# Kernel tuning notes

Measured on AMD Instinct MI355X. Metric: run time of the kernel, lower is better.

## Reference

```python
import jax, jax.numpy as jnp
import numpy as np

B, S, D, H = 4, 2048, 1024, 16
DK = D // H

def setup_inputs() -> dict:
    key = jax.random.key(0)
    ks = jax.random.split(key, 11)
    sc = 1.0 / np.sqrt(D)
    return {
        "query": jax.random.normal(ks[0], (B, S, D), jnp.float32),
        "key_": jax.random.normal(ks[1], (B, S, D), jnp.float32),
        "value": jax.random.normal(ks[2], (B, S, D), jnp.float32),
        "Wq": jax.random.normal(ks[3], (D, D), jnp.float32) * sc,
        "bq": jnp.zeros((D,), jnp.float32),
        "Wk": jax.random.normal(ks[4], (D, D), jnp.float32) * sc,
        "bk": jnp.zeros((D,), jnp.float32),
        "Wv": jax.random.normal(ks[5], (D, D), jnp.float32) * sc,
        "bv": jnp.zeros((D,), jnp.float32),
        "Wo": jax.random.normal(ks[6], (D, D), jnp.float32) * sc,
        "bo": jnp.zeros((D,), jnp.float32),
    }

def reference(query, key_, value, Wq, bq, Wk, bk, Wv, bv, Wo, bo):
    def proj(x, W, b):
        # [B,S,D] -> [B,H,S,DK]
        y = x @ W.T + b
        return y.reshape(B, S, H, DK).transpose(0, 2, 1, 3)
    q = proj(query, Wq, bq)
    k = proj(key_, Wk, bk)
    v = proj(value, Wv, bv)
    scores = jnp.einsum("bhqd,bhkd->bhqk", q, k) / jnp.sqrt(jnp.float32(DK))
    p = jax.nn.softmax(scores, axis=-1)
    x = jnp.einsum("bhqk,bhkd->bhqd", p, v)
    x = x.transpose(0, 2, 1, 3).reshape(B, S, D)
    return x @ Wo.T + bo
```

## Files before the change

kernel.cpp:

```cpp
#include <hip/hip_runtime.h>
#include <math.h>

#define Bc 4
#define Sc 2048
#define Dc 1024
#define Hc 16
#define DKc 64

#define QSCALE_L2E 0.1803368801f
#define ZINIT_L2E  -11.5415603f

typedef __bf16 bf16;
typedef __bf16 bf16x2 __attribute__((ext_vector_type(2)));
typedef __bf16 bf16x4 __attribute__((ext_vector_type(4)));
typedef __bf16 bf16x8 __attribute__((ext_vector_type(8)));
typedef float  floatx4 __attribute__((ext_vector_type(4)));
typedef float  floatx16 __attribute__((ext_vector_type(16)));

__device__ __forceinline__ void load_lds16(const void* g, void* l) {
    __builtin_amdgcn_global_load_lds((const __attribute__((address_space(1))) void*)g,
                                     (__attribute__((address_space(3))) void*)l, 16, 0, 0);
}

#define MFMA16(a, b, c) __builtin_amdgcn_mfma_f32_16x16x32_bf16(a, b, c, 0, 0, 0)
#define MFMA32(a, b, c) __builtin_amdgcn_mfma_f32_32x32x16_bf16(a, b, c, 0, 0, 0)

__device__ __forceinline__ float exp2_fast(float x) {
    float r;
    asm("v_exp_f32 %0, %1" : "=v"(r) : "v"(x));
    return r;
}


#define GSTAGE(dbuf, kk) do {                                                 \
    load_lds16(A + (size_t)(m0 + w * 16 + srow) * K + (kk) + scol,            \
               As + (dbuf) * 4096 + w * 512);                                 \
    load_lds16(W + (size_t)(n0 + w * 16 + srow) * K + (kk) + scol,            \
               Bs + (dbuf) * 4096 + w * 512);                                 \
    load_lds16(A + (size_t)(m0 + (w + 4) * 16 + srow) * K + (kk) + scol,      \
               As + (dbuf) * 4096 + (w + 4) * 512);                           \
    load_lds16(W + (size_t)(n0 + (w + 4) * 16 + srow) * K + (kk) + scol,      \
               Bs + (dbuf) * 4096 + (w + 4) * 512);                           \
} while (0)

#define GCOMP(dbuf) do {                                                      \
    const bf16* Ab = As + (dbuf) * 4096;                                      \
    const bf16* Bb = Bs + (dbuf) * 4096;                                      \
    const bf16x8 af0 = *(const bf16x8*)(Ab + (wm + fl) * 32 + fq * 8);        \
    const bf16x8 af1 = *(const bf16x8*)(Ab + (wm + 16 + fl) * 32 + fq * 8);   \
    const bf16x8 af2 = *(const bf16x8*)(Ab + (wm + 32 + fl) * 32 + fq * 8);   \
    const bf16x8 af3 = *(const bf16x8*)(Ab + (wm + 48 + fl) * 32 + fq * 8);   \
    const bf16x8 bg0 = *(const bf16x8*)(Bb + (wn + fl) * 32 + fq * 8);        \
    const bf16x8 bg1 = *(const bf16x8*)(Bb + (wn + 16 + fl) * 32 + fq * 8);   \
    const bf16x8 bg2 = *(const bf16x8*)(Bb + (wn + 32 + fl) * 32 + fq * 8);   \
    const bf16x8 bg3 = *(const bf16x8*)(Bb + (wn + 48 + fl) * 32 + fq * 8);   \
    acc[0][0] = MFMA16(af0, bg0, acc[0][0]); acc[0][1] = MFMA16(af0, bg1, acc[0][1]); \
    acc[0][2] = MFMA16(af0, bg2, acc[0][2]); acc[0][3] = MFMA16(af0, bg3, acc[0][3]); \
    acc[1][0] = MFMA16(af1, bg0, acc[1][0]); acc[1][1] = MFMA16(af1, bg1, acc[1][1]); \
    acc[1][2] = MFMA16(af1, bg2, acc[1][2]); acc[1][3] = MFMA16(af1, bg3, acc[1][3]); \
    acc[2][0] = MFMA16(af2, bg0, acc[2][0]); acc[2][1] = MFMA16(af2, bg1, acc[2][1]); \
    acc[2][2] = MFMA16(af2, bg2, acc[2][2]); acc[2][3] = MFMA16(af2, bg3, acc[2][3]); \
    acc[3][0] = MFMA16(af3, bg0, acc[3][0]); acc[3][1] = MFMA16(af3, bg1, acc[3][1]); \
    acc[3][2] = MFMA16(af3, bg2, acc[3][2]); acc[3][3] = MFMA16(af3, bg3, acc[3][3]); \
} while (0)

template<int MODE>
__device__ __forceinline__ void gemm_body(const bf16* __restrict__ A,
                                          const bf16* __restrict__ W,
                                          const float* __restrict__ bias,
                                          void* __restrict__ out,
                                          bf16* As, bf16* Bs,
                                          int m0, int n0) {
    constexpr int N = Dc, K = Dc;
    const int t  = threadIdx.x;
    const int w  = t >> 6;
    const int l  = t & 63;
    const int wm = (w >> 1) * 64;
    const int wn = (w & 1) * 64;
    const int srow = l >> 2;
    const int scol = (l & 3) * 8;
    const int fl = l & 15;
    const int fq = l >> 4;

    floatx4 acc[4][4];
#pragma unroll
    for (int i = 0; i < 4; i++)
#pragma unroll
        for (int j = 0; j < 4; j++)
            acc[i][j] = (floatx4){0.f, 0.f, 0.f, 0.f};

    GSTAGE(0, 0);
    __syncthreads();
#pragma unroll 1
    for (int k0 = 0; k0 < K; k0 += 64) {
        GSTAGE(1, k0 + 32);
        GCOMP(0);
        __syncthreads();
        if (k0 + 64 < K) GSTAGE(0, k0 + 64);
        GCOMP(1);
        __syncthreads();
    }

#pragma unroll
    for (int tn = 0; tn < 4; tn++) {
        const int n = n0 + wn + tn * 16 + fl;
        const float bv = bias[n];
#pragma unroll
        for (int tm = 0; tm < 4; tm++) {
            const int mb = m0 + wm + tm * 16 + fq * 4;
            if (MODE == 0) {
                float* O = (float*)out;
#pragma unroll
                for (int r = 0; r < 4; r++)
                    O[(size_t)(mb + r) * N + n] = acc[tm][tn][r] + bv;
            } else if (MODE == 1) {
                bf16* O = (bf16*)out;
#pragma unroll
                for (int r = 0; r < 4; r++)
                    O[(size_t)(mb + r) * N + n] = (bf16)(acc[tm][tn][r] + bv);
            } else {
                const int h = n >> 6, dk = n & 63;
                const int b = mb >> 11, s = mb & 2047;
                bf16* O = (bf16*)out + ((size_t)((b * Hc + h) * DKc + dk)) * Sc + s;
                bf16x4 pk = {(bf16)(acc[tm][tn][0] + bv), (bf16)(acc[tm][tn][1] + bv),
                             (bf16)(acc[tm][tn][2] + bv), (bf16)(acc[tm][tn][3] + bv)};
                *(bf16x4*)O = pk;
            }
        }
    }
}

__global__ __launch_bounds__(256) void gemm_qkv(
    const bf16* __restrict__ Aq, const bf16* __restrict__ Ak, const bf16* __restrict__ Av,
    const bf16* __restrict__ Wqb, const bf16* __restrict__ Wkb, const bf16* __restrict__ Wvb,
    const float* __restrict__ bqs, const float* __restrict__ bk, const float* __restrict__ bv,
    bf16* __restrict__ Oq, bf16* __restrict__ Ok, bf16* __restrict__ Ov) {
    __shared__ bf16 As[2 * 128 * 32];
    __shared__ bf16 Bs[2 * 128 * 32];
    const int bid  = blockIdx.x;
    const int xcd  = bid & 7;
    const int slot = bid >> 3;
    const int x    = slot & 7;
    const int j    = slot >> 3;
    const int yg   = xcd + 8 * j;
    const int sel  = yg >> 6;
    const int y    = yg & 63;
    const int m0 = y * 128, n0 = x * 128;
    if (sel == 0)      gemm_body<1>(Aq, Wqb, bqs, Oq, As, Bs, m0, n0);
    else if (sel == 1) gemm_body<1>(Ak, Wkb, bk,  Ok, As, Bs, m0, n0);
    else               gemm_body<2>(Av, Wvb, bv,  Ov, As, Bs, m0, n0);
}

__global__ __launch_bounds__(256) void gemm_out_k(const bf16* __restrict__ A,
                                                  const bf16* __restrict__ W,
                                                  const float* __restrict__ bias,
                                                  float* __restrict__ out) {
    __shared__ bf16 As[2 * 128 * 32];
    __shared__ bf16 Bs[2 * 128 * 32];
    const int bid  = blockIdx.x;
    const int xcd  = bid & 7;
    const int slot = bid >> 3;
    const int x    = slot & 7;
    const int j    = slot >> 3;
    const int y    = xcd + 8 * j;
    gemm_body<0>(A, W, bias, out, As, Bs, y * 128, x * 128);
}


__device__ __forceinline__ unsigned pkpair(float a, float b) {
    union { bf16x2 v; unsigned u; } x;
    x.v = (bf16x2){(bf16)a, (bf16)b};
    return x.u;
}

__device__ __forceinline__ bf16x8 frag4(unsigned a, unsigned b, unsigned c, unsigned d) {
    union { unsigned u[4]; bf16x8 v; } x;
    x.u[0] = a; x.u[1] = b; x.u[2] = c; x.u[3] = d;
    return x.v;
}

__device__ __forceinline__ floatx16 splat16(float v) {
    floatx16 r;
#pragma unroll
    for (int i = 0; i < 16; ++i) r[i] = v;
    return r;
}

#define PSWAP(x, y) do {                                                      \
    auto _r = __builtin_amdgcn_permlane32_swap((int)(x), (int)(y), false, false); \
    (x) = (unsigned)_r[0]; (y) = (unsigned)_r[1];                             \
} while (0)

#define STAGE(dst, kt) do {                                                   \
    load_lds16(Kb + (size_t)((kt) + w * 16 + r8) * Dc + c8 * 8,               \
               &Kbuf[dst][w * 1024]);                                         \
    load_lds16(Kb + (size_t)((kt) + w * 16 + 8 + r8) * Dc + c8 * 8,           \
               &Kbuf[dst][w * 1024 + 512]);                                   \
    load_lds16(Vb + (size_t)(w * 16 + r8) * Sc + (kt) + c8 * 8,               \
               &Vbuf[dst][w * 1024]);                                         \
    load_lds16(Vb + (size_t)(w * 16 + 8 + r8) * Sc + (kt) + c8 * 8,           \
               &Vbuf[dst][w * 1024 + 512]);                                   \
} while (0)

#define QKT(d, T, SACC) do {                                                  \
    const bf16* Kp = &Kbuf[d][((T) * 32 + ky) * 64];                          \
    const bf16x8 kf0 = *(const bf16x8*)(Kp + ((b5 ^ sw7) * 8));               \
    const bf16x8 kf1 = *(const bf16x8*)(Kp + (((2 + b5) ^ sw7) * 8));         \
    const bf16x8 kf2 = *(const bf16x8*)(Kp + (((4 + b5) ^ sw7) * 8));         \
    const bf16x8 kf3 = *(const bf16x8*)(Kp + (((6 + b5) ^ sw7) * 8));         \
    __builtin_amdgcn_s_setprio(1);                                            \
    SACC = MFMA32(kf0, qf0, z16);                                             \
    SACC = MFMA32(kf1, qf1, SACC);                                            \
    SACC = MFMA32(kf2, qf2, SACC);                                            \
    SACC = MFMA32(kf3, qf3, SACC);                                            \
    __builtin_amdgcn_s_setprio(0);                                            \
} while (0)

#define SOFTX(SACC, PF0, PF1) do {                                            \
    const float p0  = exp2_fast(SACC[0]),  p1  = exp2_fast(SACC[1]);          \
    const float p2  = exp2_fast(SACC[2]),  p3  = exp2_fast(SACC[3]);          \
    const float p4  = exp2_fast(SACC[4]),  p5  = exp2_fast(SACC[5]);          \
    const float p6  = exp2_fast(SACC[6]),  p7  = exp2_fast(SACC[7]);          \
    const float p8  = exp2_fast(SACC[8]),  p9  = exp2_fast(SACC[9]);          \
    const float p10 = exp2_fast(SACC[10]), p11 = exp2_fast(SACC[11]);         \
    const float p12 = exp2_fast(SACC[12]), p13 = exp2_fast(SACC[13]);         \
    const float p14 = exp2_fast(SACC[14]), p15 = exp2_fast(SACC[15]);         \
    lsum += (((p0 + p1) + (p2 + p3)) + ((p4 + p5) + (p6 + p7)))               \
          + (((p8 + p9) + (p10 + p11)) + ((p12 + p13) + (p14 + p15)));        \
    unsigned d0 = pkpair(p0, p1),   d1 = pkpair(p2, p3);                      \
    unsigned d2 = pkpair(p4, p5),   d3 = pkpair(p6, p7);                      \
    PSWAP(d0, d2); PSWAP(d1, d3);                                             \
    PF0 = frag4(d0, d1, d2, d3);                                              \
    unsigned e0 = pkpair(p8, p9),   e1 = pkpair(p10, p11);                    \
    unsigned e2 = pkpair(p12, p13), e3 = pkpair(p14, p15);                    \
    PSWAP(e0, e2); PSWAP(e1, e3);                                             \
    PF1 = frag4(e0, e1, e2, e3);                                              \
} while (0)

#define PVT(d, T, PF0, PF1) do {                                              \
    const bf16* Va = &Vbuf[d][ky * 64];                                       \
    const bf16* Vc = Va + 32 * 64;                                            \
    const bf16x8 vf00 = *(const bf16x8*)(Va + (((((T) << 2) + b5) ^ sw7) * 8));      \
    const bf16x8 vf01 = *(const bf16x8*)(Va + (((((T) << 2) + 2 + b5) ^ sw7) * 8));  \
    const bf16x8 vf10 = *(const bf16x8*)(Vc + (((((T) << 2) + b5) ^ sw7) * 8));      \
    const bf16x8 vf11 = *(const bf16x8*)(Vc + (((((T) << 2) + 2 + b5) ^ sw7) * 8));  \
    __builtin_amdgcn_s_setprio(1);                                            \
    oa = MFMA32(vf00, PF0, oa);                                               \
    oa = MFMA32(vf01, PF1, oa);                                               \
    ob = MFMA32(vf10, PF0, ob);                                               \
    ob = MFMA32(vf11, PF1, ob);                                               \
    __builtin_amdgcn_s_setprio(0);                                            \
} while (0)

#define REGION(d) do {                                                        \
    QKT(d, 0, sacc0);                                                         \
    QKT(d, 1, sacc1);                                                         \
    SOFTX(sacc0, pa0, pa1);                                                   \
    PVT(d, 0, pa0, pa1);                                                      \
    SOFTX(sacc1, pb0, pb1);                                                   \
    PVT(d, 1, pb0, pb1);                                                      \
} while (0)

__global__ __launch_bounds__(256, 3) void attn_mfma(const bf16* __restrict__ Q,
                                                    const bf16* __restrict__ Kg,
                                                    const bf16* __restrict__ Vt,
                                                    bf16* __restrict__ X) {
    __shared__ bf16 Kbuf[2][64 * 64];
    __shared__ bf16 Vbuf[2][64 * 64];

    const int bh = blockIdx.x & 63;
    const int qb = blockIdx.x >> 6;
    const int b = bh >> 4, h = bh & 15;

    const int w   = threadIdx.x >> 6;
    const int l   = threadIdx.x & 63;
    const int ky  = l & 31;
    const int b5  = l >> 5;
    const int sw7 = l & 7;
    const int r8  = l >> 3;
    const int c8  = (l & 7) ^ r8;
    const int q0i = qb * 128 + w * 32;

    const bf16* Qb = Q  + (size_t)b * Sc * Dc + h * DKc;
    const bf16* Kb = Kg + (size_t)b * Sc * Dc + h * DKc;
    const bf16* Vb = Vt + (size_t)((b * Hc + h) * DKc) * Sc;

    const bf16* Qrow = Qb + (size_t)(q0i + ky) * Dc + 8 * b5;
    const bf16x8 qf0 = *(const bf16x8*)(Qrow);
    const bf16x8 qf1 = *(const bf16x8*)(Qrow + 16);
    const bf16x8 qf2 = *(const bf16x8*)(Qrow + 32);
    const bf16x8 qf3 = *(const bf16x8*)(Qrow + 48);

    const floatx16 z16 = splat16(ZINIT_L2E);
    floatx16 oa = splat16(0.f), ob = splat16(0.f);
    floatx16 sacc0, sacc1;
    bf16x8 pa0, pa1, pb0, pb1;
    float lsum = 0.f;

    STAGE(0, 0);
    __syncthreads();

#pragma unroll 1
    for (int kt = 0; kt < Sc; kt += 128) {
        STAGE(1, kt + 64);
        REGION(0);
        __syncthreads();
        if (kt + 128 < Sc) STAGE(0, kt + 128);
        REGION(1);
        __syncthreads();
    }

    lsum += __shfl_xor(lsum, 32);
    const float inv = 1.f / lsum;
    bf16* xp = X + ((size_t)(b * Sc + q0i + ky)) * Dc + h * DKc + b5 * 4;
#pragma unroll
    for (int g = 0; g < 4; ++g) {
        bf16x4 pa = {(bf16)(oa[4 * g + 0] * inv), (bf16)(oa[4 * g + 1] * inv),
                     (bf16)(oa[4 * g + 2] * inv), (bf16)(oa[4 * g + 3] * inv)};
        *(bf16x4*)(xp + g * 8) = pa;
        bf16x4 pb = {(bf16)(ob[4 * g + 0] * inv), (bf16)(ob[4 * g + 1] * inv),
                     (bf16)(ob[4 * g + 2] * inv), (bf16)(ob[4 * g + 3] * inv)};
        *(bf16x4*)(xp + 32 + g * 8) = pb;
    }
}

__global__ __launch_bounds__(256) void prep(
    const float* __restrict__ q, const float* __restrict__ k, const float* __restrict__ v,
    const float* __restrict__ wq, const float* __restrict__ wk,
    const float* __restrict__ wv, const float* __restrict__ wo,
    const float* __restrict__ bq,
    bf16* __restrict__ oq, bf16* __restrict__ ok, bf16* __restrict__ ov,
    bf16* __restrict__ w0, bf16* __restrict__ w1,
    bf16* __restrict__ w2, bf16* __restrict__ w3,
    float* __restrict__ bqs) {
    const int NQ = 3 * 8192;
    const int NW = 4 * 1024;
    int bid = blockIdx.x;
    if (bid < NQ) {
        const int sel = bid >> 13;
        const int i = (bid & 8191) * 256 + threadIdx.x;
        const float* src = sel == 0 ? q : sel == 1 ? k : v;
        bf16* dst = sel == 0 ? oq : sel == 1 ? ok : ov;
        const float4 vv = ((const float4*)src)[i];
        bf16x4 o = {(bf16)vv.x, (bf16)vv.y, (bf16)vv.z, (bf16)vv.w};
        ((bf16x4*)dst)[i] = o;
    } else if (bid < NQ + NW) {
        bid -= NQ;
        const int sel = bid >> 10;
        const int i = (bid & 1023) * 256 + threadIdx.x;
        const float* src = sel == 0 ? wq : sel == 1 ? wk : sel == 2 ? wv : wo;
        bf16* dst = sel == 0 ? w0 : sel == 1 ? w1 : sel == 2 ? w2 : w3;
        const float scale = sel == 0 ? QSCALE_L2E : 1.f;
        const float4 vv = ((const float4*)src)[i];
        bf16x4 o = {(bf16)(vv.x * scale), (bf16)(vv.y * scale),
                    (bf16)(vv.z * scale), (bf16)(vv.w * scale)};
        ((bf16x4*)dst)[i] = o;
    } else {
        const int i = (bid - NQ - NW) * 256 + threadIdx.x;
        if (i < Dc) bqs[i] = bq[i] * QSCALE_L2E;
    }
}

extern "C" void kernel_launch(void* const* d_in, const int* in_sizes, int n_in,
                              void* d_out, int out_size, void* d_ws, size_t ws_size,
                              hipStream_t stream) {
    const float* query = (const float*)d_in[0];
    const float* key_  = (const float*)d_in[1];
    const float* value = (const float*)d_in[2];
    const float* Wq    = (const float*)d_in[3];
    const float* bq    = (const float*)d_in[4];
    const float* Wk    = (const float*)d_in[5];
    const float* bk    = (const float*)d_in[6];
    const float* Wv    = (const float*)d_in[7];
    const float* bv    = (const float*)d_in[8];
    const float* Wo    = (const float*)d_in[9];
    const float* bo    = (const float*)d_in[10];

    const size_t nSD = (size_t)Bc * Sc * Dc;
    const size_t nWW = (size_t)Dc * Dc;

    char* ws = (char*)d_ws;
    bf16* qbf = (bf16*)ws;              ws += nSD * 2;
    bf16* kbf = (bf16*)ws;              ws += nSD * 2;
    bf16* vbf = (bf16*)ws;              ws += nSD * 2;
    bf16* wqb = (bf16*)ws;              ws += nWW * 2;
    bf16* wkb = (bf16*)ws;              ws += nWW * 2;
    bf16* wvb = (bf16*)ws;              ws += nWW * 2;
    bf16* wob = (bf16*)ws;              ws += nWW * 2;
    bf16* Qw  = (bf16*)ws;              ws += nSD * 2;
    bf16* Kw  = (bf16*)ws;              ws += nSD * 2;
    bf16* Vtw = (bf16*)ws;              ws += nSD * 2;
    bf16* Xw  = (bf16*)ws;              ws += nSD * 2;
    float* bqs = (float*)ws;            ws += Dc * 4;

    prep<<<3 * 8192 + 4 * 1024 + 4, 256, 0, stream>>>(
        query, key_, value, Wq, Wk, Wv, Wo, bq,
        qbf, kbf, vbf, wqb, wkb, wvb, wob, bqs);

    gemm_qkv<<<3 * (Bc * Sc / 128) * (Dc / 128), 256, 0, stream>>>(
        qbf, kbf, vbf, wqb, wkb, wvb, bqs, bk, bv, Qw, Kw, Vtw);

    attn_mfma<<<(Sc / 128) * Hc * Bc, 256, 0, stream>>>(Qw, Kw, Vtw, Xw);

    gemm_out_k<<<(Bc * Sc / 128) * (Dc / 128), 256, 0, stream>>>(
        Xw, wob, bo, (float*)d_out);
}
```

Before: 343.1 us.

## Triple-buffer GEMM LDS staging with one barrier per k-step

```diff
diff --git a/kernel.cpp b/kernel.cpp
--- a/kernel.cpp
+++ b/kernel.cpp
@@ -32,20 +32,20 @@
 }
 
 
-#define GSTAGE(dbuf, kk) do {                                                 \
+#define GSTAGE(slot, kk) do {                                                 \
     load_lds16(A + (size_t)(m0 + w * 16 + srow) * K + (kk) + scol,            \
-               As + (dbuf) * 4096 + w * 512);                                 \
+               As + (slot) * 4096 + w * 512);                                 \
     load_lds16(W + (size_t)(n0 + w * 16 + srow) * K + (kk) + scol,            \
-               Bs + (dbuf) * 4096 + w * 512);                                 \
+               Bs + (slot) * 4096 + w * 512);                                 \
     load_lds16(A + (size_t)(m0 + (w + 4) * 16 + srow) * K + (kk) + scol,      \
-               As + (dbuf) * 4096 + (w + 4) * 512);                           \
+               As + (slot) * 4096 + (w + 4) * 512);                           \
     load_lds16(W + (size_t)(n0 + (w + 4) * 16 + srow) * K + (kk) + scol,      \
-               Bs + (dbuf) * 4096 + (w + 4) * 512);                           \
-} while (0)
-
-#define GCOMP(dbuf) do {                                                      \
-    const bf16* Ab = As + (dbuf) * 4096;                                      \
-    const bf16* Bb = Bs + (dbuf) * 4096;                                      \
+               Bs + (slot) * 4096 + (w + 4) * 512);                           \
+} while (0)
+
+#define GCOMP(slot) do {                                                      \
+    const bf16* Ab = As + (slot) * 4096;                                      \
+    const bf16* Bb = Bs + (slot) * 4096;                                      \
     const bf16x8 af0 = *(const bf16x8*)(Ab + (wm + fl) * 32 + fq * 8);        \
     const bf16x8 af1 = *(const bf16x8*)(Ab + (wm + 16 + fl) * 32 + fq * 8);   \
     const bf16x8 af2 = *(const bf16x8*)(Ab + (wm + 32 + fl) * 32 + fq * 8);   \
@@ -90,16 +90,18 @@
             acc[i][j] = (floatx4){0.f, 0.f, 0.f, 0.f};
 
     GSTAGE(0, 0);
+    GSTAGE(1, 32);
+
+#pragma unroll 1
+    for (int s = 0; s < 31; ++s) {
+        asm volatile("s_waitcnt vmcnt(4)" ::: "memory");
+        __builtin_amdgcn_s_barrier();
+        __builtin_amdgcn_sched_barrier(0);
+        if (s + 2 < 32) GSTAGE((s + 2) % 3, 32 * (s + 2));
+        GCOMP(s % 3);
+    }
     __syncthreads();
-#pragma unroll 1
-    for (int k0 = 0; k0 < K; k0 += 64) {
-        GSTAGE(1, k0 + 32);
-        GCOMP(0);
-        __syncthreads();
-        if (k0 + 64 < K) GSTAGE(0, k0 + 64);
-        GCOMP(1);
-        __syncthreads();
-    }
+    GCOMP(1);
 
 #pragma unroll
     for (int tn = 0; tn < 4; tn++) {
@@ -120,8 +122,8 @@
                     O[(size_t)(mb + r) * N + n] = (bf16)(acc[tm][tn][r] + bv);
             } else {
                 const int h = n >> 6, dk = n & 63;
-                const int b = mb >> 11, s = mb & 2047;
-                bf16* O = (bf16*)out + ((size_t)((b * Hc + h) * DKc + dk)) * Sc + s;
+                const int b = mb >> 11, s2 = mb & 2047;
+                bf16* O = (bf16*)out + ((size_t)((b * Hc + h) * DKc + dk)) * Sc + s2;
                 bf16x4 pk = {(bf16)(acc[tm][tn][0] + bv), (bf16)(acc[tm][tn][1] + bv),
                              (bf16)(acc[tm][tn][2] + bv), (bf16)(acc[tm][tn][3] + bv)};
                 *(bf16x4*)O = pk;
@@ -135,8 +137,8 @@
     const bf16* __restrict__ Wqb, const bf16* __restrict__ Wkb, const bf16* __restrict__ Wvb,
     const float* __restrict__ bqs, const float* __restrict__ bk, const float* __restrict__ bv,
     bf16* __restrict__ Oq, bf16* __restrict__ Ok, bf16* __restrict__ Ov) {
-    __shared__ bf16 As[2 * 128 * 32];
-    __shared__ bf16 Bs[2 * 128 * 32];
+    __shared__ bf16 As[3 * 128 * 32];
+    __shared__ bf16 Bs[3 * 128 * 32];
     const int bid  = blockIdx.x;
     const int xcd  = bid & 7;
     const int slot = bid >> 3;
@@ -155,8 +157,8 @@
                                                   const bf16* __restrict__ W,
                                                   const float* __restrict__ bias,
                                                   float* __restrict__ out) {
-    __shared__ bf16 As[2 * 128 * 32];
-    __shared__ bf16 Bs[2 * 128 * 32];
+    __shared__ bf16 As[3 * 128 * 32];
+    __shared__ bf16 Bs[3 * 128 * 32];
     const int bid  = blockIdx.x;
     const int xcd  = bid & 7;
     const int slot = bid >> 3;
```

Result: faster. 328.8 us (-4.2%).
